# Kernel optimization log

Hardware: AMD Instinct MI355X
Metric: run time of the kernel (lower is better)

## Reference

```python
import jax, jax.numpy as jnp
import numpy as np

N_NODES = 100000
N_EDGES = 1600000
IN_FEAT = 128
UNITS = 64


def setup_inputs() -> dict:
    key = jax.random.key(0)
    k1, k2, k3, k4, k5 = jax.random.split(key, 5)
    node_states = jax.random.normal(k1, (N_NODES, IN_FEAT), dtype=jnp.float32)
    # edges[:,0] is the destination/segment id; the original TF code's
    # repeat(bincount) normalization assumes edges sorted by edges[:,0].
    dst = jnp.sort(jax.random.randint(k2, (N_EDGES,), 0, N_NODES))
    src = jax.random.randint(k3, (N_EDGES,), 0, N_NODES)
    edges = jnp.stack([dst, src], axis=1).astype(jnp.int64)
    kernel = jax.random.normal(k4, (IN_FEAT, UNITS), dtype=jnp.float32) * 0.05
    kernel_attention = jax.random.normal(k5, (2 * UNITS, 1), dtype=jnp.float32) * 0.05
    return {"node_states": node_states, "edges": edges,
            "kernel": kernel, "kernel_attention": kernel_attention}


def reference(node_states, edges, kernel, kernel_attention):
    n_nodes = node_states.shape[0]
    dst = edges[:, 0]  # segment ids (aggregation target)
    src = edges[:, 1]  # neighbor being gathered

    h = node_states @ kernel                      # [N, U]
    h_dst = h[dst]                                # [E, U]
    h_src = h[src]                                # [E, U]
    # concat(h_dst, h_src) @ a  ==  h_dst @ a[:U] + h_src @ a[U:]
    u = kernel_attention.shape[0] // 2
    scores = (h_dst @ kernel_attention[:u] + h_src @ kernel_attention[u:])[:, 0]  # [E]
    scores = jax.nn.leaky_relu(scores, negative_slope=0.2)  # tf default alpha=0.2
    scores = jnp.exp(jnp.clip(scores, -2.0, 2.0))

    score_sum = jax.ops.segment_sum(scores, dst, num_segments=n_nodes)  # [N]
    attn = scores / score_sum[dst]                                      # [E]

    out = jax.ops.segment_sum(h_src * attn[:, None], dst, num_segments=n_nodes)  # [N, U]
    return out
```

## Files before the change

### kernel.cpp

```cpp
#include <hip/hip_runtime.h>
#include <hip/hip_bf16.h>

#define NN 100000
#define NE 1600000
#define NF 128
#define UU 64

typedef __attribute__((ext_vector_type(8))) short short8;
typedef __attribute__((ext_vector_type(4))) float f32x4;
typedef __attribute__((ext_vector_type(2))) float f32x2;
typedef __attribute__((ext_vector_type(4))) unsigned u32x4;

static const size_t OFF_FLAG = 0;
static const size_t OFF_H2   = 256;
static const size_t OFF_AD   = OFF_H2  + (size_t)NN * UU * 2;
static const size_t OFF_AS   = OFF_AD  + (size_t)NN * 4;
static const size_t OFF_ROW  = OFF_AS  + (size_t)NN * 4;
static const size_t OFF_WP   = OFF_ROW + (size_t)(NN + 1) * 4;

__device__ __forceinline__ unsigned short bfr(float v) {
    unsigned u = __float_as_uint(v);
    return (unsigned short)((u + 0x7FFFu + ((u >> 16) & 1u)) >> 16);
}

__device__ __forceinline__ unsigned cvtpk(float lo, float hi) {
    unsigned r;
    asm("v_cvt_pk_bf16_f32 %0, %1, %2" : "=v"(r) : "v"(lo), "v"(hi));
    return r;
}

__device__ __forceinline__ void pkfma(f32x2& acc, unsigned w32, float s) {
    f32x2 p, s2;
    p.x = __uint_as_float(w32 << 16);
    p.y = __uint_as_float(w32 & 0xFFFF0000u);
    s2.x = s; s2.y = s;
    acc = __builtin_elementwise_fma(p, s2, acc);
}

__global__ __launch_bounds__(256) void prep(const int* __restrict__ ew,
                                            const float* __restrict__ W,
                                            int* __restrict__ flag,
                                            unsigned short* __restrict__ Wp) {
    if (blockIdx.x == 0) {
        if (threadIdx.x == 0) {
            int a = ew[2 * 400000 + 1] | ew[2 * 800000 + 1] |
                    ew[2 * 1200000 + 1] | ew[2 * 1599999 + 1];
            *flag = (a == 0) ? 1 : 0;
        }
        return;
    }
    int i = (blockIdx.x - 1) * 256 + threadIdx.x;
    int j   = i & 7;
    int l15 = (i >> 3) & 15;
    int quad = (i >> 7) & 3;
    int kb  = (i >> 9) & 3;
    int nt  = i >> 11;
    Wp[i] = bfr(W[(size_t)(kb * 32 + quad * 8 + j) * UU + nt * 16 + l15]);
}

#define GEMM_BLOCKS   1563
#define ROWS_BLOCKS   391

__global__ __launch_bounds__(256) void mega(const float* __restrict__ X,
                                            const void* __restrict__ edges,
                                            const int* __restrict__ flag,
                                            const unsigned short* __restrict__ Wp,
                                            const float* __restrict__ ka,
                                            unsigned short* __restrict__ h2,
                                            float* __restrict__ a_dst,
                                            float* __restrict__ a_src,
                                            int* __restrict__ rows) {
    int bid = blockIdx.x;
    int tid = threadIdx.x;

    if (bid < GEMM_BLOCKS) {
        int wv = tid >> 6, lane = tid & 63;
        int quad = lane >> 4, l15 = lane & 15;
        int nb = bid * 64 + wv * 16;
        int row = nb + l15; if (row >= NN) row = NN - 1;
        const float* xr = X + (size_t)row * NF + quad * 8;

        short8 afrag[4];
#pragma unroll
        for (int kb = 0; kb < 4; kb++) {
            float4 p0 = *(const float4*)(xr + kb * 32);
            float4 p1 = *(const float4*)(xr + kb * 32 + 4);
            u32x4 aw;
            aw[0] = cvtpk(p0.x, p0.y); aw[1] = cvtpk(p0.z, p0.w);
            aw[2] = cvtpk(p1.x, p1.y); aw[3] = cvtpk(p1.z, p1.w);
            afrag[kb] = __builtin_bit_cast(short8, aw);
        }

        f32x4 acc[4] = {f32x4{0,0,0,0}, f32x4{0,0,0,0}, f32x4{0,0,0,0}, f32x4{0,0,0,0}};
        const short8* wpf = (const short8*)Wp;
#pragma unroll
        for (int nt = 0; nt < 4; nt++) {
#pragma unroll
            for (int kb = 0; kb < 4; kb++) {
                short8 b = wpf[((nt * 4 + kb) * 4 + quad) * 16 + l15];
                acc[nt] = __builtin_amdgcn_mfma_f32_16x16x32_bf16(afrag[kb], b, acc[nt], 0, 0, 0);
            }
        }

        float kad[4], kas[4];
#pragma unroll
        for (int nt = 0; nt < 4; nt++) {
            kad[nt] = ka[nt * 16 + l15];
            kas[nt] = ka[64 + nt * 16 + l15];
        }
#pragma unroll
        for (int r = 0; r < 4; r++) {
            int m = nb + quad * 4 + r;
            if (m < NN) {
#pragma unroll
                for (int nt = 0; nt < 4; nt++) {
                    unsigned v = cvtpk(acc[nt][r], acc[nt][r]);
                    h2[(size_t)m * UU + nt * 16 + l15] = (unsigned short)v;
                }
            }
            float pd = acc[0][r] * kad[0] + acc[1][r] * kad[1] + acc[2][r] * kad[2] + acc[3][r] * kad[3];
            float ps = acc[0][r] * kas[0] + acc[1][r] * kas[1] + acc[2][r] * kas[2] + acc[3][r] * kas[3];
            pd += __shfl_xor(pd, 1); pd += __shfl_xor(pd, 2);
            pd += __shfl_xor(pd, 4); pd += __shfl_xor(pd, 8);
            ps += __shfl_xor(ps, 1); ps += __shfl_xor(ps, 2);
            ps += __shfl_xor(ps, 4); ps += __shfl_xor(ps, 8);
            if (l15 == 0 && m < NN) { a_dst[m] = pd; a_src[m] = ps; }
        }
        return;
    }
    bid -= GEMM_BLOCKS;

    {
        int n = bid * 256 + tid;
        if (n > NN) return;
        if (n == NN) { rows[NN] = NE; return; }
        int fl = *flag;
        const int* ew = (const int*)edges;
        int lo = 0, hi = NE;
        while (lo < hi) {
            int mid = (lo + hi) >> 1;
            int d = fl ? ew[4 * (size_t)mid] : ew[2 * (size_t)mid];
            if (d < n) lo = mid + 1; else hi = mid;
        }
        rows[n] = lo;
    }
}

__device__ __forceinline__ float edge_score(float ad, float as) {
    float sc = ad + as;
    sc = sc > 0.f ? sc : 0.2f * sc;
    sc = fminf(fmaxf(sc, -2.f), 2.f);
    return __expf(sc);
}

__global__ __launch_bounds__(256) void aggregate(const void* __restrict__ edges,
                                                 const int* __restrict__ flag,
                                                 const int* __restrict__ rows,
                                                 const float* __restrict__ a_dst,
                                                 const float* __restrict__ a_src,
                                                 const unsigned short* __restrict__ h2,
                                                 float* __restrict__ out) {
    int tid = threadIdx.x;
    int lane = tid & 63;
    int g = lane >> 4, gl = lane & 15;
    int n = blockIdx.x * 16 + (tid >> 6) * 4 + g;
    if (n >= NN) return;
    int s = rows[n], e = rows[n + 1];
    int cnt = e - s;
    float ad = a_dst[n];
    int fl = *flag;
    const int* ew = (const int*)edges;
    const int* sp = ew + (fl ? 2 : 1);
    int lsh = fl ? 2 : 1;
    const unsigned short* h2g = h2 + gl * 4;
    int gbase = g * 16;
    f32x2 acc01 = f32x2{0.f, 0.f};
    f32x2 acc23 = f32x2{0.f, 0.f};
    float inv;

#define BATCH(MS, MW, BOFF)                                                  \
    {                                                                        \
        uint2 rr[4]; float sw[4]; int sjv[4];                                \
        _Pragma("unroll")                                                    \
        for (int t = 0; t < 4; t++) {                                        \
            sjv[t] = __shfl(MS, gbase + (BOFF) + t);                         \
            sw[t]  = __shfl(MW, gbase + (BOFF) + t);                         \
        }                                                                    \
        _Pragma("unroll")                                                    \
        for (int t = 0; t < 4; t++)                                          \
            rr[t] = *(const uint2*)(h2g + (size_t)sjv[t] * UU);              \
        _Pragma("unroll")                                                    \
        for (int t = 0; t < 4; t++) {                                        \
            pkfma(acc01, rr[t].x, sw[t]);                                    \
            pkfma(acc23, rr[t].y, sw[t]);                                    \
        }                                                                    \
    }

    if (cnt <= 64) {
        int msrc[4];
#pragma unroll
        for (int k = 0; k < 4; k++) {
            int c = k * 16 + gl;
            msrc[k] = (c < cnt) ? sp[(size_t)(s + c) << lsh] : 0;
        }
        int sjv0[2][4];
#pragma unroll
        for (int b = 0; b < 2; b++)
#pragma unroll
            for (int t = 0; t < 4; t++)
                sjv0[b][t] = __shfl(msrc[0], gbase + b * 4 + t);
        uint2 rr0[2][4];
#pragma unroll
        for (int b = 0; b < 2; b++)
#pragma unroll
            for (int t = 0; t < 4; t++)
                rr0[b][t] = *(const uint2*)(h2g + (size_t)sjv0[b][t] * UU);
        float mw[4];
#pragma unroll
        for (int k = 0; k < 4; k++) {
            int c = k * 16 + gl;
            mw[k] = (c < cnt) ? edge_score(ad, a_src[msrc[k]]) : 0.f;
        }
#pragma unroll
        for (int b = 0; b < 2; b++) {
#pragma unroll
            for (int t = 0; t < 4; t++) {
                float w = __shfl(mw[0], gbase + b * 4 + t);
                pkfma(acc01, rr0[b][t].x, w);
                pkfma(acc23, rr0[b][t].y, w);
            }
        }
#pragma unroll
        for (int b = 2; b < 4; b++) {
            if (b * 4 < cnt) BATCH(msrc[0], mw[0], b * 4);
        }
#pragma unroll
        for (int k = 1; k < 4; k++) {
#pragma unroll
            for (int b = 0; b < 4; b++) {
                if (k * 16 + b * 4 < cnt) BATCH(msrc[k], mw[k], b * 4);
            }
        }
        float t0 = (mw[0] + mw[1]) + (mw[2] + mw[3]);
        t0 += __shfl_xor(t0, 1); t0 += __shfl_xor(t0, 2);
        t0 += __shfl_xor(t0, 4); t0 += __shfl_xor(t0, 8);
        inv = (cnt > 0) ? 1.f / t0 : 0.f;
    } else {
        float t0 = 0.f;
        for (int c = gl; c < cnt; c += 16) {
            int sj = sp[(size_t)(s + c) << lsh];
            t0 += edge_score(ad, a_src[sj]);
        }
        t0 += __shfl_xor(t0, 1); t0 += __shfl_xor(t0, 2);
        t0 += __shfl_xor(t0, 4); t0 += __shfl_xor(t0, 8);
        inv = 1.f / t0;
        for (int c0 = 0; c0 < cnt; c0 += 16) {
            int c = c0 + gl;
            int sj = 0; float w = 0.f;
            if (c < cnt) {
                sj = sp[(size_t)(s + c) << lsh];
                w = edge_score(ad, a_src[sj]);
            }
#pragma unroll
            for (int b = 0; b < 4; b++) {
                if (c0 + b * 4 < cnt) BATCH(sj, w, b * 4);
            }
        }
    }
#undef BATCH

    float4 o;
    o.x = acc01.x * inv; o.y = acc01.y * inv;
    o.z = acc23.x * inv; o.w = acc23.y * inv;
    *(float4*)(out + (size_t)n * UU + gl * 4) = o;
}

extern "C" void kernel_launch(void* const* d_in, const int* in_sizes, int n_in,
                              void* d_out, int out_size, void* d_ws, size_t ws_size,
                              hipStream_t stream) {
    const float* X  = (const float*)d_in[0];
    const void*  Ed = d_in[1];
    const float* W  = (const float*)d_in[2];
    const float* KA = (const float*)d_in[3];
    float* out = (float*)d_out;

    char* ws = (char*)d_ws;
    int*            flag  = (int*)(ws + OFF_FLAG);
    unsigned short* h2    = (unsigned short*)(ws + OFF_H2);
    float*          a_dst = (float*)(ws + OFF_AD);
    float*          a_src = (float*)(ws + OFF_AS);
    int*            rows  = (int*)(ws + OFF_ROW);
    unsigned short* Wp    = (unsigned short*)(ws + OFF_WP);

    prep<<<33, 256, 0, stream>>>((const int*)Ed, W, flag, Wp);
    mega<<<GEMM_BLOCKS + ROWS_BLOCKS, 256, 0, stream>>>(
        X, Ed, flag, Wp, KA, h2, a_dst, a_src, rows);
    aggregate<<<(NN + 15) / 16, 256, 0, stream>>>(Ed, flag, rows, a_dst, a_src, h2, out);
}
```

Baseline: 144.1 us.

## Fold weight-packing prep kernel into GEMM blocks and permute h2 column layout

```diff
diff --git a/kernel.cpp b/kernel.cpp
--- a/kernel.cpp
+++ b/kernel.cpp
@@ -11,17 +11,10 @@
 typedef __attribute__((ext_vector_type(2))) float f32x2;
 typedef __attribute__((ext_vector_type(4))) unsigned u32x4;
 
-static const size_t OFF_FLAG = 0;
-static const size_t OFF_H2   = 256;
+static const size_t OFF_H2   = 0;
 static const size_t OFF_AD   = OFF_H2  + (size_t)NN * UU * 2;
 static const size_t OFF_AS   = OFF_AD  + (size_t)NN * 4;
 static const size_t OFF_ROW  = OFF_AS  + (size_t)NN * 4;
-static const size_t OFF_WP   = OFF_ROW + (size_t)(NN + 1) * 4;
-
-__device__ __forceinline__ unsigned short bfr(float v) {
-    unsigned u = __float_as_uint(v);
-    return (unsigned short)((u + 0x7FFFu + ((u >> 16) & 1u)) >> 16);
-}
 
 __device__ __forceinline__ unsigned cvtpk(float lo, float hi) {
     unsigned r;
@@ -37,25 +30,10 @@
     acc = __builtin_elementwise_fma(p, s2, acc);
 }
 
-__global__ __launch_bounds__(256) void prep(const int* __restrict__ ew,
-                                            const float* __restrict__ W,
-                                            int* __restrict__ flag,
-                                            unsigned short* __restrict__ Wp) {
-    if (blockIdx.x == 0) {
-        if (threadIdx.x == 0) {
-            int a = ew[2 * 400000 + 1] | ew[2 * 800000 + 1] |
-                    ew[2 * 1200000 + 1] | ew[2 * 1599999 + 1];
-            *flag = (a == 0) ? 1 : 0;
-        }
-        return;
-    }
-    int i = (blockIdx.x - 1) * 256 + threadIdx.x;
-    int j   = i & 7;
-    int l15 = (i >> 3) & 15;
-    int quad = (i >> 7) & 3;
-    int kb  = (i >> 9) & 3;
-    int nt  = i >> 11;
-    Wp[i] = bfr(W[(size_t)(kb * 32 + quad * 8 + j) * UU + nt * 16 + l15]);
+__device__ __forceinline__ int edge_flag(const int* ew) {
+    int a = ew[2 * 400000 + 1] | ew[2 * 800000 + 1] |
+            ew[2 * 1200000 + 1] | ew[2 * 1599999 + 1];
+    return (a == 0) ? 1 : 0;
 }
 
 #define GEMM_BLOCKS   1563
@@ -63,13 +41,13 @@
 
 __global__ __launch_bounds__(256) void mega(const float* __restrict__ X,
                                             const void* __restrict__ edges,
-                                            const int* __restrict__ flag,
-                                            const unsigned short* __restrict__ Wp,
+                                            const float* __restrict__ W,
                                             const float* __restrict__ ka,
                                             unsigned short* __restrict__ h2,
                                             float* __restrict__ a_dst,
                                             float* __restrict__ a_src,
                                             int* __restrict__ rows) {
+    __shared__ unsigned Wl[4096];
     int bid = blockIdx.x;
     int tid = threadIdx.x;
 
@@ -80,24 +58,46 @@
         int row = nb + l15; if (row >= NN) row = NN - 1;
         const float* xr = X + (size_t)row * NF + quad * 8;
 
+        float4 p0[4], p1[4];
+#pragma unroll
+        for (int kb = 0; kb < 4; kb++) {
+            p0[kb] = *(const float4*)(xr + kb * 32);
+            p1[kb] = *(const float4*)(xr + kb * 32 + 4);
+        }
+
+#pragma unroll
+        for (int it = 0; it < 16; it++) {
+            int d = it * 256 + tid;
+            int i0 = d * 2;
+            int j  = i0 & 7;
+            int l  = (i0 >> 3) & 15;
+            int q  = (i0 >> 7) & 3;
+            int kb = (i0 >> 9) & 3;
+            int nt = i0 >> 11;
+            int r0 = kb * 32 + q * 8 + j;
+            int c  = nt * 16 + l;
+            float w0 = W[(size_t)r0 * UU + c];
+            float w1 = W[(size_t)(r0 + 1) * UU + c];
+            Wl[d] = cvtpk(w0, w1);
+        }
+
         short8 afrag[4];
 #pragma unroll
         for (int kb = 0; kb < 4; kb++) {
-            float4 p0 = *(const float4*)(xr + kb * 32);
-            float4 p1 = *(const float4*)(xr + kb * 32 + 4);
             u32x4 aw;
-            aw[0] = cvtpk(p0.x, p0.y); aw[1] = cvtpk(p0.z, p0.w);
-            aw[2] = cvtpk(p1.x, p1.y); aw[3] = cvtpk(p1.z, p1.w);
+            aw[0] = cvtpk(p0[kb].x, p0[kb].y); aw[1] = cvtpk(p0[kb].z, p0[kb].w);
+            aw[2] = cvtpk(p1[kb].x, p1[kb].y); aw[3] = cvtpk(p1[kb].z, p1[kb].w);
             afrag[kb] = __builtin_bit_cast(short8, aw);
         }
+        __syncthreads();
 
         f32x4 acc[4] = {f32x4{0,0,0,0}, f32x4{0,0,0,0}, f32x4{0,0,0,0}, f32x4{0,0,0,0}};
-        const short8* wpf = (const short8*)Wp;
+        const short8* wl8 = (const short8*)Wl;
 #pragma unroll
         for (int nt = 0; nt < 4; nt++) {
 #pragma unroll
             for (int kb = 0; kb < 4; kb++) {
-                short8 b = wpf[((nt * 4 + kb) * 4 + quad) * 16 + l15];
+                short8 b = wl8[((nt * 4 + kb) * 4 + quad) * 16 + l15];
                 acc[nt] = __builtin_amdgcn_mfma_f32_16x16x32_bf16(afrag[kb], b, acc[nt], 0, 0, 0);
             }
         }
@@ -112,11 +112,10 @@
         for (int r = 0; r < 4; r++) {
             int m = nb + quad * 4 + r;
             if (m < NN) {
-#pragma unroll
-                for (int nt = 0; nt < 4; nt++) {
-                    unsigned v = cvtpk(acc[nt][r], acc[nt][r]);
-                    h2[(size_t)m * UU + nt * 16 + l15] = (unsigned short)v;
-                }
+                uint2 v;
+                v.x = cvtpk(acc[0][r], acc[1][r]);
+                v.y = cvtpk(acc[2][r], acc[3][r]);
+                *(uint2*)(h2 + (size_t)m * UU + l15 * 4) = v;
             }
             float pd = acc[0][r] * kad[0] + acc[1][r] * kad[1] + acc[2][r] * kad[2] + acc[3][r] * kad[3];
             float ps = acc[0][r] * kas[0] + acc[1][r] * kas[1] + acc[2][r] * kas[2] + acc[3][r] * kas[3];
@@ -133,9 +132,9 @@
     {
         int n = bid * 256 + tid;
         if (n > NN) return;
+        const int* ew = (const int*)edges;
         if (n == NN) { rows[NN] = NE; return; }
-        int fl = *flag;
-        const int* ew = (const int*)edges;
+        int fl = edge_flag(ew);
         int lo = 0, hi = NE;
         while (lo < hi) {
             int mid = (lo + hi) >> 1;
@@ -154,7 +153,6 @@
 }
 
 __global__ __launch_bounds__(256) void aggregate(const void* __restrict__ edges,
-                                                 const int* __restrict__ flag,
                                                  const int* __restrict__ rows,
                                                  const float* __restrict__ a_dst,
                                                  const float* __restrict__ a_src,
@@ -168,8 +166,8 @@
     int s = rows[n], e = rows[n + 1];
     int cnt = e - s;
     float ad = a_dst[n];
-    int fl = *flag;
     const int* ew = (const int*)edges;
+    int fl = edge_flag(ew);
     const int* sp = ew + (fl ? 2 : 1);
     int lsh = fl ? 2 : 1;
     const unsigned short* h2g = h2 + gl * 4;
@@ -269,10 +267,11 @@
     }
 #undef BATCH
 
-    float4 o;
-    o.x = acc01.x * inv; o.y = acc01.y * inv;
-    o.z = acc23.x * inv; o.w = acc23.y * inv;
-    *(float4*)(out + (size_t)n * UU + gl * 4) = o;
+    float* outr = out + (size_t)n * UU + gl;
+    outr[0]  = acc01.x * inv;
+    outr[16] = acc01.y * inv;
+    outr[32] = acc23.x * inv;
+    outr[48] = acc23.y * inv;
 }
 
 extern "C" void kernel_launch(void* const* d_in, const int* in_sizes, int n_in,
@@ -285,15 +284,12 @@
     float* out = (float*)d_out;
 
     char* ws = (char*)d_ws;
-    int*            flag  = (int*)(ws + OFF_FLAG);
     unsigned short* h2    = (unsigned short*)(ws + OFF_H2);
     float*          a_dst = (float*)(ws + OFF_AD);
     float*          a_src = (float*)(ws + OFF_AS);
     int*            rows  = (int*)(ws + OFF_ROW);
-    unsigned short* Wp    = (unsigned short*)(ws + OFF_WP);
-
-    prep<<<33, 256, 0, stream>>>((const int*)Ed, W, flag, Wp);
+
     mega<<<GEMM_BLOCKS + ROWS_BLOCKS, 256, 0, stream>>>(
-        X, Ed, flag, Wp, KA, h2, a_dst, a_src, rows);
-    aggregate<<<(NN + 15) / 16, 256, 0, stream>>>(Ed, flag, rows, a_dst, a_src, h2, out);
-}
+        X, Ed, W, KA, h2, a_dst, a_src, rows);
+    aggregate<<<(NN + 15) / 16, 256, 0, stream>>>(Ed, rows, a_dst, a_src, h2, out);
+}
```

Result: no change. 143.0 us (-0.8%).
